# Kernel tuning notes

Hardware: AMD Instinct MI355X
Metric: run time of the kernel (lower is better)

## Reference

```python
import jax, jax.numpy as jnp
import numpy as np

T, B, D, N = 2048, 16, 1024, 128
EPS = 1e-6


def setup_inputs() -> dict:
    key = jax.random.key(0)
    ks = jax.random.split(key, 6)
    sc = 1.0 / np.sqrt(D)  # ~xavier scale for [N, D] projections
    x = jax.random.normal(ks[0], (T, B, D), jnp.float32)
    S = jnp.zeros((B, N, N), jnp.float32)
    W_k = jax.random.normal(ks[1], (N, D), jnp.float32) * sc
    W_v = jax.random.normal(ks[2], (N, D), jnp.float32) * sc
    W_q = jax.random.normal(ks[3], (N, D), jnp.float32) * sc
    W_beta = jax.random.normal(ks[4], (N, D), jnp.float32) * sc
    d_beta = jnp.full((N,), 0.1, jnp.float32)
    b_beta = jnp.zeros((N,), jnp.float32)
    return {"x": x, "S": S, "W_k": W_k, "W_v": W_v, "W_q": W_q,
            "W_beta": W_beta, "d_beta": d_beta, "b_beta": b_beta}


def reference(x, S, W_k, W_v, W_q, W_beta, d_beta, b_beta):
    # Batched input projections (dense GEMMs over all T*B tokens at once).
    k_all = jnp.einsum('tbd,nd->tbn', x, W_k)
    v_all = jnp.einsum('tbd,nd->tbn', x, W_v)
    q_all = jnp.einsum('tbd,nd->tbn', x, W_q)
    bx_all = jnp.einsum('tbd,nd->tbn', x, W_beta)

    def step(S, inp):
        k, v, q, bx = inp  # each [B, N]
        k_norm = k / (jnp.linalg.norm(k, axis=-1, keepdims=True) + EPS)
        retrieved = jnp.einsum('bij,bj->bi', S, k_norm)
        beta = jax.nn.sigmoid(bx + d_beta * retrieved + b_beta)
        # Delta rule: S += beta * outer(v - retrieved, k_norm)
        S = S + beta[..., None] * ((v - retrieved)[..., None] * k_norm[:, None, :])
        out = jnp.einsum('bij,bj->bi', S, q)
        out = out * jax.nn.silu(out)  # self-gated output
        return S, out

    S_final, outputs = jax.lax.scan(step, S, (k_all, v_all, q_all, bx_all))
    return outputs, S_final
```

## Files before the change

### kernel.cpp

```cpp
#include <hip/hip_runtime.h>
#include <hip/hip_bf16.h>


#define T_STEPS 2048
#define NB 16
#define ND 128
#define KD 1024
#define PSTRIDE 512

typedef __attribute__((ext_vector_type(4))) float f32x4;
typedef __attribute__((ext_vector_type(8))) short short8v;

__device__ __forceinline__ unsigned short f2bf(float f) {
  union { float f; unsigned int u; } c; c.f = f;
  unsigned int u = c.u;
  unsigned int r = u + 0x7fffu + ((u >> 16) & 1u);
  return (unsigned short)(r >> 16);
}

__global__ __launch_bounds__(256) void proj_gemm(
    const float* __restrict__ X,
    const float* __restrict__ Wk, const float* __restrict__ Wv,
    const float* __restrict__ Wq, const float* __restrict__ Wb,
    float* __restrict__ C)
{
  __shared__ unsigned short As[128 * 64];
  __shared__ unsigned short Bs[128 * 64];
  const int tid = threadIdx.x;
  const int bm = blockIdx.x;
  const int bn = blockIdx.y;
  const float* W = (bn == 0) ? Wk : ((bn == 1) ? Wv : ((bn == 2) ? Wq : Wb));
  const int lane = tid & 63;
  const int wave = tid >> 6;
  const int wr = wave >> 1, wc = wave & 1;

  f32x4 acc[4][4];
#pragma unroll
  for (int i = 0; i < 4; i++)
#pragma unroll
    for (int j = 0; j < 4; j++) acc[i][j] = (f32x4){0.f, 0.f, 0.f, 0.f};

  for (int k0 = 0; k0 < KD; k0 += 64) {
    __syncthreads();
#pragma unroll
    for (int c = 0; c < 4; c++) {
      const int g = tid + c * 256;
      const int row = g >> 3;
      const int ch = g & 7;
      const int pos = ((ch ^ (row & 7)) * 8);
      {
        const float* ga = X + (size_t)(bm * 128 + row) * KD + k0 + ch * 8;
        float4 f0 = *(const float4*)(ga);
        float4 f1 = *(const float4*)(ga + 4);
        union { unsigned short u[8]; short8v v; } pk2;
        pk2.u[0] = f2bf(f0.x); pk2.u[1] = f2bf(f0.y);
        pk2.u[2] = f2bf(f0.z); pk2.u[3] = f2bf(f0.w);
        pk2.u[4] = f2bf(f1.x); pk2.u[5] = f2bf(f1.y);
        pk2.u[6] = f2bf(f1.z); pk2.u[7] = f2bf(f1.w);
        *reinterpret_cast<short8v*>(&As[row * 64 + pos]) = pk2.v;
      }
      {
        const float* gb = W + (size_t)row * KD + k0 + ch * 8;
        float4 f0 = *(const float4*)(gb);
        float4 f1 = *(const float4*)(gb + 4);
        union { unsigned short u[8]; short8v v; } pk2;
        pk2.u[0] = f2bf(f0.x); pk2.u[1] = f2bf(f0.y);
        pk2.u[2] = f2bf(f0.z); pk2.u[3] = f2bf(f0.w);
        pk2.u[4] = f2bf(f1.x); pk2.u[5] = f2bf(f1.y);
        pk2.u[6] = f2bf(f1.z); pk2.u[7] = f2bf(f1.w);
        *reinterpret_cast<short8v*>(&Bs[row * 64 + pos]) = pk2.v;
      }
    }
    __syncthreads();
#pragma unroll
    for (int kk = 0; kk < 2; kk++) {
      const int ch = kk * 4 + (lane >> 4);
      short8v a[4], b[4];
#pragma unroll
      for (int i = 0; i < 4; i++) {
        const int ar = wr * 64 + i * 16 + (lane & 15);
        a[i] = *reinterpret_cast<const short8v*>(&As[ar * 64 + ((ch ^ (ar & 7)) * 8)]);
        const int br = wc * 64 + i * 16 + (lane & 15);
        b[i] = *reinterpret_cast<const short8v*>(&Bs[br * 64 + ((ch ^ (br & 7)) * 8)]);
      }
#pragma unroll
      for (int i = 0; i < 4; i++)
#pragma unroll
        for (int j = 0; j < 4; j++)
          acc[i][j] = __builtin_amdgcn_mfma_f32_16x16x32_bf16(a[i], b[j], acc[i][j], 0, 0, 0);
    }
  }
#pragma unroll
  for (int i = 0; i < 4; i++)
#pragma unroll
    for (int j = 0; j < 4; j++)
#pragma unroll
      for (int r = 0; r < 4; r++) {
        const int row = bm * 128 + wr * 64 + i * 16 + (lane >> 4) * 4 + r;
        const int col = bn * 128 + wc * 64 + j * 16 + (lane & 15);
        C[(size_t)row * PSTRIDE + col] = acc[i][j][r];
      }
}

__global__ __launch_bounds__(256) void norm_k(float* __restrict__ proj) {
  const int lane = threadIdx.x & 63;
  const int wid = (blockIdx.x * 256 + threadIdx.x) >> 6;
  float* rowp = proj + (size_t)wid * PSTRIDE;
  float2 kv = *reinterpret_cast<float2*>(rowp + lane * 2);
  float ss = kv.x * kv.x + kv.y * kv.y;
  ss += __shfl_xor(ss, 1);
  ss += __shfl_xor(ss, 2);
  ss += __shfl_xor(ss, 4);
  ss += __shfl_xor(ss, 8);
  ss += __shfl_xor(ss, 16);
  ss += __shfl_xor(ss, 32);
  const float rn = 1.0f / (sqrtf(ss) + 1e-6f);
  kv.x *= rn; kv.y *= rn;
  *reinterpret_cast<float2*>(rowp + lane * 2) = kv;
}

__device__ __forceinline__ float sum8d(float v) {
  v += __int_as_float(__builtin_amdgcn_update_dpp(0, __float_as_int(v), 0xB1, 0xF, 0xF, true));
  v += __int_as_float(__builtin_amdgcn_update_dpp(0, __float_as_int(v), 0x4E, 0xF, 0xF, true));
  v += __int_as_float(__builtin_amdgcn_update_dpp(0, __float_as_int(v), 0x128, 0xF, 0xF, true));
  return v;
}

struct Buf { f32x4 kn[4]; f32x4 q[4]; float v, bx; };

__device__ __forceinline__ void load_buf(const float* __restrict__ p, int c, int row, Buf& b) {
  const f32x4* p4 = reinterpret_cast<const f32x4*>(p);
#pragma unroll
  for (int j = 0; j < 4; j++) b.kn[j] = p4[c * 4 + j];
#pragma unroll
  for (int j = 0; j < 4; j++) b.q[j] = p4[64 + c * 4 + j];
  b.v = p[128 + row];
  b.bx = p[384 + row];
}

__device__ __forceinline__ float core(const Buf& b, float db, float bb, f32x4 S4[4]) {
  f32x4 a0 = S4[0] * b.kn[0];
  f32x4 a1 = S4[1] * b.kn[1];
  a0 = __builtin_elementwise_fma(S4[2], b.kn[2], a0);
  a1 = __builtin_elementwise_fma(S4[3], b.kn[3], a1);
  const f32x4 acc = a0 + a1;
  const float r = sum8d((acc.x + acc.y) + (acc.z + acc.w));
  const float lg = fmaf(db, r, b.bx + bb);
  const float beta = __builtin_amdgcn_rcpf(1.0f + __expf(-lg));
  const float cr = beta * (b.v - r);
  const f32x4 cr4 = {cr, cr, cr, cr};
#pragma unroll
  for (int j = 0; j < 4; j++) S4[j] = __builtin_elementwise_fma(cr4, b.kn[j], S4[j]);
  f32x4 o0 = S4[0] * b.q[0];
  f32x4 o1 = S4[1] * b.q[1];
  o0 = __builtin_elementwise_fma(S4[2], b.q[2], o0);
  o1 = __builtin_elementwise_fma(S4[3], b.q[3], o1);
  const f32x4 ao = o0 + o1;
  return sum8d((ao.x + ao.y) + (ao.z + ao.w));
}

__device__ __forceinline__ float fin(float od) {
  return od * od * __builtin_amdgcn_rcpf(1.0f + __expf(-od));
}

__global__ __launch_bounds__(64) void scan_kernel(
    const float* __restrict__ proj, const float* __restrict__ S_in,
    const float* __restrict__ d_beta, const float* __restrict__ b_beta,
    float* __restrict__ out, float* __restrict__ S_out)
{
  const int lane = threadIdx.x & 63;
  const int batch = blockIdx.x & 15;
  const int wv = blockIdx.x >> 4;
  const int c = (lane & 3) | ((lane & 8) >> 1);
  const int rloc = ((lane >> 2) & 1) | (((lane >> 4) & 3) << 1);
  const int row = wv * 8 + rloc;
  const bool w0 = ((lane & 11) == 0);

  f32x4 S4[4];
  {
    const f32x4* Sp4 = reinterpret_cast<const f32x4*>(
        S_in + ((size_t)batch * ND + row) * ND + c * 16);
#pragma unroll
    for (int j = 0; j < 4; j++) S4[j] = Sp4[j];
  }
  const float db = d_beta[row];
  const float bb = b_beta[row];

  const float* pb = proj + (size_t)batch * PSTRIDE;
  const size_t sstep = (size_t)NB * PSTRIDE;
  float* outp = out + (size_t)batch * ND + row;
  const size_t ostep = (size_t)NB * ND;

  Buf A, B, C, D;
  __builtin_amdgcn_sched_barrier(0);
  load_buf(pb + 0 * sstep, c, row, A);
  load_buf(pb + 1 * sstep, c, row, B);
  load_buf(pb + 2 * sstep, c, row, C);
  load_buf(pb + 3 * sstep, c, row, D);
  __builtin_amdgcn_sched_barrier(0);

  float od_prev;

#define SLOT(BUF, tnext)                                                  \
  do {                                                                    \
    const float gprev = fin(od_prev);                                     \
    if (w0) *outp = gprev;                                                \
    outp += ostep;                                                        \
    od_prev = core(BUF, db, bb, S4);                                      \
    __builtin_amdgcn_sched_barrier(0);                                    \
    load_buf(pb + (size_t)(tnext) * sstep, c, row, BUF);                  \
    __builtin_amdgcn_sched_barrier(0);                                    \
  } while (0)

  od_prev = core(A, db, bb, S4);
  __builtin_amdgcn_sched_barrier(0);
  load_buf(pb + 4 * sstep, c, row, A);
  __builtin_amdgcn_sched_barrier(0);
  SLOT(B, 5);
  SLOT(C, 6);
  SLOT(D, 7);

  for (int t = 4; t < T_STEPS; t += 4) {
    const int t4 = (t + 4 < T_STEPS) ? t + 4 : T_STEPS - 1;
    const int t5 = (t + 5 < T_STEPS) ? t + 5 : T_STEPS - 1;
    const int t6 = (t + 6 < T_STEPS) ? t + 6 : T_STEPS - 1;
    const int t7 = (t + 7 < T_STEPS) ? t + 7 : T_STEPS - 1;
    SLOT(A, t4);
    SLOT(B, t5);
    SLOT(C, t6);
    SLOT(D, t7);
  }
  {
    const float g = fin(od_prev);
    if (w0) *outp = g;
  }
#undef SLOT

  {
    f32x4* So4 = reinterpret_cast<f32x4*>(
        S_out + ((size_t)batch * ND + row) * ND + c * 16);
#pragma unroll
    for (int j = 0; j < 4; j++) So4[j] = S4[j];
  }
}

extern "C" void kernel_launch(void* const* d_in, const int* in_sizes, int n_in,
                              void* d_out, int out_size, void* d_ws, size_t ws_size,
                              hipStream_t stream) {
  const float* x  = (const float*)d_in[0];
  const float* S0 = (const float*)d_in[1];
  const float* Wk = (const float*)d_in[2];
  const float* Wv = (const float*)d_in[3];
  const float* Wq = (const float*)d_in[4];
  const float* Wb = (const float*)d_in[5];
  const float* db = (const float*)d_in[6];
  const float* bb = (const float*)d_in[7];
  float* out  = (float*)d_out;
  float* Sout = out + (size_t)T_STEPS * NB * ND;
  float* proj = (float*)d_ws;

  dim3 ggrid(256, 4);
  proj_gemm<<<ggrid, 256, 0, stream>>>(x, Wk, Wv, Wq, Wb, proj);
  norm_k<<<8192, 256, 0, stream>>>(proj);
  scan_kernel<<<256, 64, 0, stream>>>(proj, S0, db, bb, out, Sout);
}
```

Measured before the change: 488.4 us.

## Split scan state across twice as many waves with 16-lane row reductions

The scan kernel now gives each lane 8 columns of S instead of 16. Each row is spread over 16 lanes and each wave covers 4 rows, so the grid doubles from 256 to 512 single-wave blocks. This halves the serial per-step FMA chain and register load, and the added parallelism can run on more CUs. In exchange, each row reduction needs an extra ds_swizzle step, and each wave makes more redundant loads of k and q for its rows.

```diff
diff --git a/kernel.cpp b/kernel.cpp
--- a/kernel.cpp
+++ b/kernel.cpp
@@ -9,6 +9,7 @@
 #define PSTRIDE 512
 
 typedef __attribute__((ext_vector_type(4))) float f32x4;
+typedef __attribute__((ext_vector_type(2))) float f32x2;
 typedef __attribute__((ext_vector_type(8))) short short8v;
 
 __device__ __forceinline__ unsigned short f2bf(float f) {
@@ -119,44 +120,51 @@
   *reinterpret_cast<float2*>(rowp + lane * 2) = kv;
 }
 
-__device__ __forceinline__ float sum8d(float v) {
+__device__ __forceinline__ float sum16d(float v) {
   v += __int_as_float(__builtin_amdgcn_update_dpp(0, __float_as_int(v), 0xB1, 0xF, 0xF, true));
   v += __int_as_float(__builtin_amdgcn_update_dpp(0, __float_as_int(v), 0x4E, 0xF, 0xF, true));
   v += __int_as_float(__builtin_amdgcn_update_dpp(0, __float_as_int(v), 0x128, 0xF, 0xF, true));
+  v += __int_as_float(__builtin_amdgcn_ds_swizzle(__float_as_int(v), 0x101F));
   return v;
 }
 
-struct Buf { f32x4 kn[4]; f32x4 q[4]; float v, bx; };
-
-__device__ __forceinline__ void load_buf(const float* __restrict__ p, int c, int row, Buf& b) {
+struct Buf { f32x4 kn[2]; f32x4 q[2]; float v, bx; };
+
+__device__ __forceinline__ void load_buf(const float* __restrict__ p, int cc, int row, Buf& b) {
   const f32x4* p4 = reinterpret_cast<const f32x4*>(p);
-#pragma unroll
-  for (int j = 0; j < 4; j++) b.kn[j] = p4[c * 4 + j];
-#pragma unroll
-  for (int j = 0; j < 4; j++) b.q[j] = p4[64 + c * 4 + j];
-  b.v = p[128 + row];
+  b.kn[0] = p4[cc * 2 + 0];
+  b.kn[1] = p4[cc * 2 + 1];
+  b.q[0]  = p4[64 + cc * 2 + 0];
+  b.q[1]  = p4[64 + cc * 2 + 1];
+  b.v  = p[128 + row];
   b.bx = p[384 + row];
 }
 
-__device__ __forceinline__ float core(const Buf& b, float db, float bb, f32x4 S4[4]) {
-  f32x4 a0 = S4[0] * b.kn[0];
-  f32x4 a1 = S4[1] * b.kn[1];
-  a0 = __builtin_elementwise_fma(S4[2], b.kn[2], a0);
-  a1 = __builtin_elementwise_fma(S4[3], b.kn[3], a1);
-  const f32x4 acc = a0 + a1;
-  const float r = sum8d((acc.x + acc.y) + (acc.z + acc.w));
+__device__ __forceinline__ float core(const Buf& b, float db, float bb, f32x2 S2[4]) {
+  const f32x2 k0 = {b.kn[0].x, b.kn[0].y}, k1 = {b.kn[0].z, b.kn[0].w};
+  const f32x2 k2 = {b.kn[1].x, b.kn[1].y}, k3 = {b.kn[1].z, b.kn[1].w};
+  f32x2 a0 = S2[0] * k0;
+  f32x2 a1 = S2[1] * k1;
+  a0 = __builtin_elementwise_fma(S2[2], k2, a0);
+  a1 = __builtin_elementwise_fma(S2[3], k3, a1);
+  const f32x2 ac = a0 + a1;
+  const float r = sum16d(ac.x + ac.y);
   const float lg = fmaf(db, r, b.bx + bb);
   const float beta = __builtin_amdgcn_rcpf(1.0f + __expf(-lg));
   const float cr = beta * (b.v - r);
-  const f32x4 cr4 = {cr, cr, cr, cr};
-#pragma unroll
-  for (int j = 0; j < 4; j++) S4[j] = __builtin_elementwise_fma(cr4, b.kn[j], S4[j]);
-  f32x4 o0 = S4[0] * b.q[0];
-  f32x4 o1 = S4[1] * b.q[1];
-  o0 = __builtin_elementwise_fma(S4[2], b.q[2], o0);
-  o1 = __builtin_elementwise_fma(S4[3], b.q[3], o1);
-  const f32x4 ao = o0 + o1;
-  return sum8d((ao.x + ao.y) + (ao.z + ao.w));
+  const f32x2 cr2 = {cr, cr};
+  S2[0] = __builtin_elementwise_fma(cr2, k0, S2[0]);
+  S2[1] = __builtin_elementwise_fma(cr2, k1, S2[1]);
+  S2[2] = __builtin_elementwise_fma(cr2, k2, S2[2]);
+  S2[3] = __builtin_elementwise_fma(cr2, k3, S2[3]);
+  const f32x2 q0 = {b.q[0].x, b.q[0].y}, q1 = {b.q[0].z, b.q[0].w};
+  const f32x2 q2 = {b.q[1].x, b.q[1].y}, q3 = {b.q[1].z, b.q[1].w};
+  f32x2 o0 = S2[0] * q0;
+  f32x2 o1 = S2[1] * q1;
+  o0 = __builtin_elementwise_fma(S2[2], q2, o0);
+  o1 = __builtin_elementwise_fma(S2[3], q3, o1);
+  const f32x2 ao = o0 + o1;
+  return sum16d(ao.x + ao.y);
 }
 
 __device__ __forceinline__ float fin(float od) {
@@ -170,18 +178,19 @@
 {
   const int lane = threadIdx.x & 63;
   const int batch = blockIdx.x & 15;
-  const int wv = blockIdx.x >> 4;
-  const int c = (lane & 3) | ((lane & 8) >> 1);
-  const int rloc = ((lane >> 2) & 1) | (((lane >> 4) & 3) << 1);
-  const int row = wv * 8 + rloc;
-  const bool w0 = ((lane & 11) == 0);
-
-  f32x4 S4[4];
+  const int grp = blockIdx.x >> 4;
+  const int cc = lane & 15;
+  const int rloc = lane >> 4;
+  const int row = grp * 4 + rloc;
+  const bool w0 = (cc == 0);
+
+  f32x2 S2[4];
   {
     const f32x4* Sp4 = reinterpret_cast<const f32x4*>(
-        S_in + ((size_t)batch * ND + row) * ND + c * 16);
-#pragma unroll
-    for (int j = 0; j < 4; j++) S4[j] = Sp4[j];
+        S_in + ((size_t)batch * ND + row) * ND + cc * 8);
+    const f32x4 s0 = Sp4[0], s1 = Sp4[1];
+    S2[0] = (f32x2){s0.x, s0.y}; S2[1] = (f32x2){s0.z, s0.w};
+    S2[2] = (f32x2){s1.x, s1.y}; S2[3] = (f32x2){s1.z, s1.w};
   }
   const float db = d_beta[row];
   const float bb = b_beta[row];
@@ -193,10 +202,10 @@
 
   Buf A, B, C, D;
   __builtin_amdgcn_sched_barrier(0);
-  load_buf(pb + 0 * sstep, c, row, A);
-  load_buf(pb + 1 * sstep, c, row, B);
-  load_buf(pb + 2 * sstep, c, row, C);
-  load_buf(pb + 3 * sstep, c, row, D);
+  load_buf(pb + 0 * sstep, cc, row, A);
+  load_buf(pb + 1 * sstep, cc, row, B);
+  load_buf(pb + 2 * sstep, cc, row, C);
+  load_buf(pb + 3 * sstep, cc, row, D);
   __builtin_amdgcn_sched_barrier(0);
 
   float od_prev;
@@ -206,15 +215,15 @@
     const float gprev = fin(od_prev);                                     \
     if (w0) *outp = gprev;                                                \
     outp += ostep;                                                        \
-    od_prev = core(BUF, db, bb, S4);                                      \
+    od_prev = core(BUF, db, bb, S2);                                      \
     __builtin_amdgcn_sched_barrier(0);                                    \
-    load_buf(pb + (size_t)(tnext) * sstep, c, row, BUF);                  \
+    load_buf(pb + (size_t)(tnext) * sstep, cc, row, BUF);                 \
     __builtin_amdgcn_sched_barrier(0);                                    \
   } while (0)
 
-  od_prev = core(A, db, bb, S4);
-  __builtin_amdgcn_sched_barrier(0);
-  load_buf(pb + 4 * sstep, c, row, A);
+  od_prev = core(A, db, bb, S2);
+  __builtin_amdgcn_sched_barrier(0);
+  load_buf(pb + 4 * sstep, cc, row, A);
   __builtin_amdgcn_sched_barrier(0);
   SLOT(B, 5);
   SLOT(C, 6);
@@ -238,9 +247,11 @@
 
   {
     f32x4* So4 = reinterpret_cast<f32x4*>(
-        S_out + ((size_t)batch * ND + row) * ND + c * 16);
-#pragma unroll
-    for (int j = 0; j < 4; j++) So4[j] = S4[j];
+        S_out + ((size_t)batch * ND + row) * ND + cc * 8);
+    f32x4 s0, s1;
+    s0.x = S2[0].x; s0.y = S2[0].y; s0.z = S2[1].x; s0.w = S2[1].y;
+    s1.x = S2[2].x; s1.y = S2[2].y; s1.z = S2[3].x; s1.w = S2[3].y;
+    So4[0] = s0; So4[1] = s1;
   }
 }
 
@@ -262,5 +273,5 @@
   dim3 ggrid(256, 4);
   proj_gemm<<<ggrid, 256, 0, stream>>>(x, Wk, Wv, Wq, Wb, proj);
   norm_k<<<8192, 256, 0, stream>>>(proj);
-  scan_kernel<<<256, 64, 0, stream>>>(proj, S0, db, bb, out, Sout);
-}
+  scan_kernel<<<512, 64, 0, stream>>>(proj, S0, db, bb, out, Sout);
+}
```

Result: slower. 511.9 us (+4.8%).
